# Performance work log

Hardware: AMD Instinct MI355X
Metric: run time of the kernel (lower is better)

Reference implementation:

```python
import jax, jax.numpy as jnp
import numpy as np

B, S, D, H = 2, 2048, 1024, 16
DEPTH = D // H

def setup_inputs() -> dict:
    key = jax.random.key(0)
    k1, k2, k3 = jax.random.split(key, 3)
    x = jax.random.normal(k1, (B, S, D), dtype=jnp.float32)
    # causal mask (1 = attend, 0 = blocked), broadcastable over batch/heads
    mask = jnp.tril(jnp.ones((S, S), dtype=jnp.int32))[None, None]
    W_qkv = jax.random.normal(k2, (D, 3 * D), dtype=jnp.float32) * (D ** -0.5)
    b_qkv = jnp.zeros((3 * D,), dtype=jnp.float32)
    W_out = jax.random.normal(k3, (D, D), dtype=jnp.float32) * (D ** -0.5)
    b_out = jnp.zeros((D,), dtype=jnp.float32)
    return {"x": x, "mask": mask, "W_qkv": W_qkv, "b_qkv": b_qkv,
            "W_out": W_out, "b_out": b_out}

def reference(x, mask, W_qkv, b_qkv, W_out, b_out):
    b, s, _ = x.shape
    qkv = x @ W_qkv + b_qkv                        # [b, s, 3D]
    qkv = qkv.reshape(b, s, H, 3 * DEPTH)          # matches torch reshape
    qkv = jnp.transpose(qkv, (0, 2, 1, 3))         # [b, h, s, 3*depth]
    q, k, v = jnp.split(qkv, 3, axis=-1)           # each [b, h, s, depth]
    scores = jnp.einsum('bhqd,bhkd->bhqk', q, k) / jnp.sqrt(jnp.float32(DEPTH))
    scores = jnp.where(mask == 0, -jnp.inf, scores)
    attn = jax.nn.softmax(scores, axis=-1)         # dropout: eval mode (identity)
    out = jnp.einsum('bhqk,bhkd->bhqd', attn, v)   # [b, h, s, depth]
    out = jnp.transpose(out, (0, 2, 1, 3)).reshape(b, s, D)
    return out @ W_out + b_out
```

## Files before the change

kernel.cpp:

```cpp
#include <hip/hip_runtime.h>

#define BB 2
#define SS 2048
#define DDIM 1024
#define HH 16
#define DEPTH 64
#define QKVN (3*DDIM)

typedef unsigned short u16;
typedef unsigned int u32;
typedef __attribute__((ext_vector_type(8))) short bf16x8;
typedef __attribute__((ext_vector_type(4))) float f32x4;

__device__ __forceinline__ u16 f2bf(float f){
  union{float f; u32 u;} z; z.f=f;
  u32 r = z.u + 0x7fffu + ((z.u>>16)&1u);
  return (u16)(r>>16);
}
#define NEG_BIG (-1e30f)

typedef const __attribute__((address_space(1))) u32* gas_t;
typedef __attribute__((address_space(3))) u32* las_t;
__device__ __forceinline__ void gl_lds16(const void* g, void* l){
  __builtin_amdgcn_global_load_lds((gas_t)g, (las_t)l, 16, 0, 0);
}

__global__ void convT_k(const float* __restrict__ in, u16* __restrict__ out, int R, int C){
  __shared__ float tile[32][33];
  int c0 = blockIdx.x<<5, r0 = blockIdx.y<<5;
  int tx = threadIdx.x, ty = threadIdx.y;
  for (int i=ty;i<32;i+=8) tile[i][tx] = in[(size_t)(r0+i)*C + c0+tx];
  __syncthreads();
  for (int i=ty;i<32;i+=8) out[(size_t)(c0+i)*R + r0+tx] = f2bf(tile[tx][i]);
}

__global__ void convX_k(const float* __restrict__ in, u16* __restrict__ out){
  size_t i = ((size_t)blockIdx.x*256 + threadIdx.x) * 8;
  float4 a = *(const float4*)(in + i);
  float4 b = *(const float4*)(in + i + 4);
  ushort4 lo = { f2bf(a.x), f2bf(a.y), f2bf(a.z), f2bf(a.w) };
  ushort4 hi = { f2bf(b.x), f2bf(b.y), f2bf(b.z), f2bf(b.w) };
  *(ushort4*)(out + i)     = lo;
  *(ushort4*)(out + i + 4) = hi;
}

__global__ __launch_bounds__(256,2) void gemm_qkv_k(
    const u16* __restrict__ A, const u16* __restrict__ Bt,
    const float* __restrict__ bias,
    u16* __restrict__ Qb, u16* __restrict__ Kb, u16* __restrict__ Vt)
{
  const int K = DDIM;
  __shared__ __align__(16) u16 As[128*32];
  __shared__ __align__(16) u16 Bs[128*32];
  const int tid = threadIdx.x;
  const int m0 = blockIdx.x<<7, n0 = blockIdx.y<<7;
  const int w = tid>>6, lane = tid&63, q = lane>>4, ln = lane&15;
  const int wr = (w>>1)<<6, wc = (w&1)<<6;

  f32x4 acc[4][4];
  #pragma unroll
  for (int i=0;i<4;i++)
    #pragma unroll
    for (int j=0;j<4;j++) acc[i][j] = (f32x4){0.f,0.f,0.f,0.f};

  for (int k0=0;k0<K;k0+=32){
    {
      int c = tid, row = c>>2, off = (c&3)<<3;
      gl_lds16(&A [(size_t)(m0+row)*K + k0 + off], &As[c<<3]);
      gl_lds16(&Bt[(size_t)(n0+row)*K + k0 + off], &Bs[c<<3]);
      c = tid + 256; row = c>>2; off = (c&3)<<3;
      gl_lds16(&A [(size_t)(m0+row)*K + k0 + off], &As[c<<3]);
      gl_lds16(&Bt[(size_t)(n0+row)*K + k0 + off], &Bs[c<<3]);
    }
    __syncthreads();
    bf16x8 af[4], bfr[4];
    #pragma unroll
    for (int i=0;i<4;i++) af[i]  = *(const bf16x8*)&As[((wr + (i<<4) + ln)<<5) + (q<<3)];
    #pragma unroll
    for (int j=0;j<4;j++) bfr[j] = *(const bf16x8*)&Bs[((wc + (j<<4) + ln)<<5) + (q<<3)];
    #pragma unroll
    for (int i=0;i<4;i++)
      #pragma unroll
      for (int j=0;j<4;j++)
        acc[i][j] = __builtin_amdgcn_mfma_f32_16x16x32_bf16(af[i], bfr[j], acc[i][j], 0, 0, 0);
    __syncthreads();
  }

  #pragma unroll
  for (int i=0;i<4;i++){
    const int mmb = m0 + wr + (i<<4) + (q<<2);
    const int bsel = mmb >> 11;
    const int sb   = mmb & 2047;
    #pragma unroll
    for (int j=0;j<4;j++){
      const int n = n0 + wc + (j<<4) + ln;
      const int h = n / 192;
      const int rr = n - h*192;
      const int bh = (bsel<<4) + h;
      const float bv = bias[n];
      if (rr < 64){
        u16* dst = Qb + (size_t)bh*SS*DEPTH + rr;
        #pragma unroll
        for (int r=0;r<4;r++) dst[(size_t)(sb+r)*DEPTH] = f2bf((acc[i][j][r] + bv)*0.125f);
      } else if (rr < 128){
        u16* dst = Kb + (size_t)bh*SS*DEPTH + (rr-64);
        #pragma unroll
        for (int r=0;r<4;r++) dst[(size_t)(sb+r)*DEPTH] = f2bf(acc[i][j][r] + bv);
      } else {
        ushort4 pv = { f2bf(acc[i][j][0] + bv), f2bf(acc[i][j][1] + bv),
                       f2bf(acc[i][j][2] + bv), f2bf(acc[i][j][3] + bv) };
        *(ushort4*)(Vt + ((size_t)bh*DEPTH + (rr-128))*SS + sb) = pv;
      }
    }
  }
}

__global__ __launch_bounds__(256,4) void attn_k(
    u16* __restrict__ Qb, const u16* __restrict__ Kb, const u16* __restrict__ Vt)
{
  __shared__ __align__(16) u16 Ks[64*64];
  __shared__ __align__(16) u16 VsT[64*64];
  __shared__ __align__(16) u16 ps[4][16*72];

  const int tid = threadIdx.x, w = tid>>6, lane = tid&63, q = lane>>4, ln = lane&15;
  const int bh = blockIdx.x;
  const int y  = blockIdx.y, sgrp = y>>3, rr_ = y&7;
  const int qt = (sgrp==0) ? 31-rr_ : (sgrp==1) ? 16+rr_ : (sgrp==2) ? 15-rr_ : rr_;
  const int r0 = qt<<6;
  const size_t kbase = (size_t)bh*SS*DEPTH;
  const size_t vbase = (size_t)bh*DEPTH*SS;

  bf16x8 qf[2];
  #pragma unroll
  for (int ks=0;ks<2;ks++)
    qf[ks] = *(const bf16x8*)(Qb + kbase + (size_t)(r0 + (w<<4) + ln)*DEPTH + (ks<<5) + (q<<3));

  f32x4 o[4];
  #pragma unroll
  for (int nt=0;nt<4;nt++) o[nt] = (f32x4){0.f,0.f,0.f,0.f};
  float m_r[4], l_r[4];
  #pragma unroll
  for (int r=0;r<4;r++){ m_r[r] = NEG_BIG; l_r[r] = 0.f; }

  const int T = qt + 1;
  for (int t=0;t<T;t++){
    __syncthreads();
    #pragma unroll
    for (int p=0;p<2;p++){
      const int e = (p*256 + tid)*8;
      gl_lds16(Kb + kbase + (size_t)(t<<6)*DEPTH + e, &Ks[e]);
      const int j = e>>6, d = e&63;
      gl_lds16(Vt + vbase + (size_t)j*SS + (t<<6) + d, &VsT[e]);
    }
    __syncthreads();

    f32x4 sc[4];
    #pragma unroll
    for (int jt=0;jt<4;jt++) sc[jt] = (f32x4){0.f,0.f,0.f,0.f};
    #pragma unroll
    for (int ks=0;ks<2;ks++){
      #pragma unroll
      for (int jt=0;jt<4;jt++){
        bf16x8 kf = *(const bf16x8*)&Ks[(((jt<<4)+ln)<<6) + (ks<<5) + (q<<3)];
        sc[jt] = __builtin_amdgcn_mfma_f32_16x16x32_bf16(qf[ks], kf, sc[jt], 0, 0, 0);
      }
    }

    if (t == T-1){
      const int rowb = r0 + (w<<4) + (q<<2);
      #pragma unroll
      for (int jt=0;jt<4;jt++){
        const int col = (t<<6) + (jt<<4) + ln;
        #pragma unroll
        for (int r=0;r<4;r++)
          if (col > rowb + r) sc[jt][r] = NEG_BIG;
      }
    }

    float alpha_r[4];
    #pragma unroll
    for (int r=0;r<4;r++){
      float mt = fmaxf(fmaxf(sc[0][r], sc[1][r]), fmaxf(sc[2][r], sc[3][r]));
      #pragma unroll
      for (int off=1; off<16; off<<=1) mt = fmaxf(mt, __shfl_xor(mt, off));
      const float mnew = fmaxf(m_r[r], mt);
      alpha_r[r] = __expf(m_r[r] - mnew);
      float p0 = __expf(sc[0][r]-mnew), p1 = __expf(sc[1][r]-mnew);
      float p2 = __expf(sc[2][r]-mnew), p3 = __expf(sc[3][r]-mnew);
      const int mrow = (q<<2) + r;
      ps[w][mrow*72 +      ln] = f2bf(p0);
      ps[w][mrow*72 + 16 + ln] = f2bf(p1);
      ps[w][mrow*72 + 32 + ln] = f2bf(p2);
      ps[w][mrow*72 + 48 + ln] = f2bf(p3);
      float psum = (p0+p1)+(p2+p3);
      #pragma unroll
      for (int off=1; off<16; off<<=1) psum += __shfl_xor(psum, off);
      l_r[r] = l_r[r]*alpha_r[r] + psum;
      m_r[r] = mnew;
    }
    #pragma unroll
    for (int nt=0;nt<4;nt++)
      #pragma unroll
      for (int r=0;r<4;r++) o[nt][r] *= alpha_r[r];

    __syncthreads();

    #pragma unroll
    for (int ks=0;ks<2;ks++){
      bf16x8 pa = *(const bf16x8*)&ps[w][ln*72 + (ks<<5) + (q<<3)];
      #pragma unroll
      for (int nt=0;nt<4;nt++){
        bf16x8 vf = *(const bf16x8*)&VsT[(((nt<<4)+ln)<<6) + (ks<<5) + (q<<3)];
        o[nt] = __builtin_amdgcn_mfma_f32_16x16x32_bf16(pa, vf, o[nt], 0, 0, 0);
      }
    }
  }

  #pragma unroll
  for (int r=0;r<4;r++){
    const float rl = 1.f / fmaxf(l_r[r], 1e-30f);
    const int s = r0 + (w<<4) + (q<<2) + r;
    #pragma unroll
    for (int nt=0;nt<4;nt++)
      Qb[kbase + (size_t)s*DEPTH + (nt<<4) + ln] = f2bf(o[nt][r] * rl);
  }
}

__global__ __launch_bounds__(256,2) void gemm_out_k(
    const u16* __restrict__ Aq, const u16* __restrict__ Bt,
    const float* __restrict__ bias, float* __restrict__ out)
{
  const int K = DDIM;
  __shared__ __align__(16) u16 As[128*32];
  __shared__ __align__(16) u16 Bs[128*32];
  const int tid = threadIdx.x;
  const int m0 = blockIdx.x<<7, n0 = blockIdx.y<<7;
  const int bsel = m0>>11, ms = m0&2047;
  const int w = tid>>6, lane = tid&63, q = lane>>4, ln = lane&15;
  const int wr = (w>>1)<<6, wc = (w&1)<<6;

  f32x4 acc[4][4];
  #pragma unroll
  for (int i=0;i<4;i++)
    #pragma unroll
    for (int j=0;j<4;j++) acc[i][j] = (f32x4){0.f,0.f,0.f,0.f};

  for (int k0=0;k0<K;k0+=32){
    const size_t abase = (size_t)((bsel<<4) + (k0>>6))*SS*DEPTH + (k0&63);
    {
      int c = tid, row = c>>2, off = (c&3)<<3;
      gl_lds16(&Aq[abase + (size_t)(ms+row)*DEPTH + off], &As[c<<3]);
      gl_lds16(&Bt[(size_t)(n0+row)*K + k0 + off],        &Bs[c<<3]);
      c = tid + 256; row = c>>2; off = (c&3)<<3;
      gl_lds16(&Aq[abase + (size_t)(ms+row)*DEPTH + off], &As[c<<3]);
      gl_lds16(&Bt[(size_t)(n0+row)*K + k0 + off],        &Bs[c<<3]);
    }
    __syncthreads();
    bf16x8 af[4], bfr[4];
    #pragma unroll
    for (int i=0;i<4;i++) af[i]  = *(const bf16x8*)&As[((wr + (i<<4) + ln)<<5) + (q<<3)];
    #pragma unroll
    for (int j=0;j<4;j++) bfr[j] = *(const bf16x8*)&Bs[((wc + (j<<4) + ln)<<5) + (q<<3)];
    #pragma unroll
    for (int i=0;i<4;i++)
      #pragma unroll
      for (int j=0;j<4;j++)
        acc[i][j] = __builtin_amdgcn_mfma_f32_16x16x32_bf16(af[i], bfr[j], acc[i][j], 0, 0, 0);
    __syncthreads();
  }

  #pragma unroll
  for (int i=0;i<4;i++){
    #pragma unroll
    for (int j=0;j<4;j++){
      const int n = n0 + wc + (j<<4) + ln;
      const float bv = bias[n];
      #pragma unroll
      for (int r=0;r<4;r++){
        const int mm = m0 + wr + (i<<4) + (q<<2) + r;
        out[(size_t)mm*DDIM + n] = acc[i][j][r] + bv;
      }
    }
  }
}

extern "C" void kernel_launch(void* const* d_in, const int* in_sizes, int n_in,
                              void* d_out, int out_size, void* d_ws, size_t ws_size,
                              hipStream_t stream)
{
  int ix = 0, iw = 2, ibq = 3, iwo = 4, ibo = 5;
  if (n_in == 5){ iw = 1; ibq = 2; iwo = 3; ibo = 4; }
  const float* x  = (const float*)d_in[ix];
  const float* Wq = (const float*)d_in[iw];
  const float* bq = (const float*)d_in[ibq];
  const float* Wo = (const float*)d_in[iwo];
  const float* bo = (const float*)d_in[ibo];
  float* out = (float*)d_out;

  u16* ws  = (u16*)d_ws;
  u16* Wqt = ws;
  u16* Wot = Wqt + (size_t)QKVN*DDIM;
  u16* Qb  = Wot + (size_t)DDIM*DDIM;
  u16* Kb  = Qb  + (size_t)BB*HH*SS*DEPTH;
  u16* Vt  = Kb  + (size_t)BB*HH*SS*DEPTH;
  u16* xb  = Vt  + (size_t)BB*HH*SS*DEPTH;

  convT_k<<<dim3(QKVN/32, DDIM/32), dim3(32,8), 0, stream>>>(Wq, Wqt, DDIM, QKVN);
  convT_k<<<dim3(DDIM/32, DDIM/32), dim3(32,8), 0, stream>>>(Wo, Wot, DDIM, DDIM);
  convX_k<<<dim3(BB*SS*DDIM/2048), 256, 0, stream>>>(x, xb);

  gemm_qkv_k<<<dim3(BB*SS/128, QKVN/128), 256, 0, stream>>>(xb, Wqt, bq, Qb, Kb, Vt);
  attn_k    <<<dim3(BB*HH, 32),           256, 0, stream>>>(Qb, Kb, Vt);
  gemm_out_k<<<dim3(BB*SS/128, DDIM/128), 256, 0, stream>>>(Qb, Wot, bo, out);
}
```

Before: 241.6 us.

## Fuse x conversion into QKV GEMM and prefetch K/V tiles in attention

Removes the separate fp32-to-bf16 conversion kernel for x by converting inside the QKV GEMM's A-tile load. In attention, the next K/V tile is prefetched into registers while the current one is computed, and LDS rows are padded to 72 elements to reduce bank conflicts. Probability tiles are also packed two bf16 values per 32-bit store using a lane shuffle. The trade-offs are more global fp32 traffic for A in every GEMM tile (x is re-read for each N block), higher register pressure, and synchronous loads replacing the async global-to-LDS copies.

```diff
diff --git a/kernel.cpp b/kernel.cpp
--- a/kernel.cpp
+++ b/kernel.cpp
@@ -34,18 +34,8 @@
   for (int i=ty;i<32;i+=8) out[(size_t)(c0+i)*R + r0+tx] = f2bf(tile[tx][i]);
 }
 
-__global__ void convX_k(const float* __restrict__ in, u16* __restrict__ out){
-  size_t i = ((size_t)blockIdx.x*256 + threadIdx.x) * 8;
-  float4 a = *(const float4*)(in + i);
-  float4 b = *(const float4*)(in + i + 4);
-  ushort4 lo = { f2bf(a.x), f2bf(a.y), f2bf(a.z), f2bf(a.w) };
-  ushort4 hi = { f2bf(b.x), f2bf(b.y), f2bf(b.z), f2bf(b.w) };
-  *(ushort4*)(out + i)     = lo;
-  *(ushort4*)(out + i + 4) = hi;
-}
-
 __global__ __launch_bounds__(256,2) void gemm_qkv_k(
-    const u16* __restrict__ A, const u16* __restrict__ Bt,
+    const float* __restrict__ Xf, const u16* __restrict__ Bt,
     const float* __restrict__ bias,
     u16* __restrict__ Qb, u16* __restrict__ Kb, u16* __restrict__ Vt)
 {
@@ -64,12 +54,15 @@
     for (int j=0;j<4;j++) acc[i][j] = (f32x4){0.f,0.f,0.f,0.f};
 
   for (int k0=0;k0<K;k0+=32){
-    {
-      int c = tid, row = c>>2, off = (c&3)<<3;
-      gl_lds16(&A [(size_t)(m0+row)*K + k0 + off], &As[c<<3]);
-      gl_lds16(&Bt[(size_t)(n0+row)*K + k0 + off], &Bs[c<<3]);
-      c = tid + 256; row = c>>2; off = (c&3)<<3;
-      gl_lds16(&A [(size_t)(m0+row)*K + k0 + off], &As[c<<3]);
+    #pragma unroll
+    for (int p=0;p<2;p++){
+      const int c = tid + (p<<8), row = c>>2, off = (c&3)<<3;
+      const float* ap = Xf + (size_t)(m0+row)*K + k0 + off;
+      float4 a0 = *(const float4*)ap, a1 = *(const float4*)(ap+4);
+      ushort4 lo = { f2bf(a0.x), f2bf(a0.y), f2bf(a0.z), f2bf(a0.w) };
+      ushort4 hi = { f2bf(a1.x), f2bf(a1.y), f2bf(a1.z), f2bf(a1.w) };
+      *(ushort4*)&As[c<<3]       = lo;
+      *(ushort4*)&As[(c<<3) + 4] = hi;
       gl_lds16(&Bt[(size_t)(n0+row)*K + k0 + off], &Bs[c<<3]);
     }
     __syncthreads();
@@ -118,8 +111,8 @@
 __global__ __launch_bounds__(256,4) void attn_k(
     u16* __restrict__ Qb, const u16* __restrict__ Kb, const u16* __restrict__ Vt)
 {
-  __shared__ __align__(16) u16 Ks[64*64];
-  __shared__ __align__(16) u16 VsT[64*64];
+  __shared__ __align__(16) u16 Ks[64*72];
+  __shared__ __align__(16) u16 VsT[64*72];
   __shared__ __align__(16) u16 ps[4][16*72];
 
   const int tid = threadIdx.x, w = tid>>6, lane = tid&63, q = lane>>4, ln = lane&15;
@@ -142,17 +135,36 @@
   #pragma unroll
   for (int r=0;r<4;r++){ m_r[r] = NEG_BIG; l_r[r] = 0.f; }
 
+  uint4 kreg[2], vreg[2];
+  #pragma unroll
+  for (int p=0;p<2;p++){
+    const int e = (p*256 + tid)*8;
+    const int j = e>>6, d = e&63;
+    kreg[p] = *(const uint4*)(Kb + kbase + e);
+    vreg[p] = *(const uint4*)(Vt + vbase + (size_t)j*SS + d);
+  }
+
   const int T = qt + 1;
   for (int t=0;t<T;t++){
     __syncthreads();
     #pragma unroll
     for (int p=0;p<2;p++){
       const int e = (p*256 + tid)*8;
-      gl_lds16(Kb + kbase + (size_t)(t<<6)*DEPTH + e, &Ks[e]);
       const int j = e>>6, d = e&63;
-      gl_lds16(Vt + vbase + (size_t)j*SS + (t<<6) + d, &VsT[e]);
-    }
-    __syncthreads();
+      *(uint4*)&Ks[j*72 + d]  = kreg[p];
+      *(uint4*)&VsT[j*72 + d] = vreg[p];
+    }
+    __syncthreads();
+
+    if (t+1 < T){
+      #pragma unroll
+      for (int p=0;p<2;p++){
+        const int e = (p*256 + tid)*8;
+        const int j = e>>6, d = e&63;
+        kreg[p] = *(const uint4*)(Kb + kbase + (size_t)((t+1)<<6)*DEPTH + e);
+        vreg[p] = *(const uint4*)(Vt + vbase + (size_t)j*SS + ((t+1)<<6) + d);
+      }
+    }
 
     f32x4 sc[4];
     #pragma unroll
@@ -161,7 +173,7 @@
     for (int ks=0;ks<2;ks++){
       #pragma unroll
       for (int jt=0;jt<4;jt++){
-        bf16x8 kf = *(const bf16x8*)&Ks[(((jt<<4)+ln)<<6) + (ks<<5) + (q<<3)];
+        bf16x8 kf = *(const bf16x8*)&Ks[((jt<<4)+ln)*72 + (ks<<5) + (q<<3)];
         sc[jt] = __builtin_amdgcn_mfma_f32_16x16x32_bf16(qf[ks], kf, sc[jt], 0, 0, 0);
       }
     }
@@ -185,14 +197,17 @@
       for (int off=1; off<16; off<<=1) mt = fmaxf(mt, __shfl_xor(mt, off));
       const float mnew = fmaxf(m_r[r], mt);
       alpha_r[r] = __expf(m_r[r] - mnew);
-      float p0 = __expf(sc[0][r]-mnew), p1 = __expf(sc[1][r]-mnew);
-      float p2 = __expf(sc[2][r]-mnew), p3 = __expf(sc[3][r]-mnew);
       const int mrow = (q<<2) + r;
-      ps[w][mrow*72 +      ln] = f2bf(p0);
-      ps[w][mrow*72 + 16 + ln] = f2bf(p1);
-      ps[w][mrow*72 + 32 + ln] = f2bf(p2);
-      ps[w][mrow*72 + 48 + ln] = f2bf(p3);
-      float psum = (p0+p1)+(p2+p3);
+      float psum = 0.f;
+      #pragma unroll
+      for (int jt=0;jt<4;jt++){
+        const float p = __expf(sc[jt][r] - mnew);
+        psum += p;
+        const u32 myv = (u32)f2bf(p);
+        const u32 ov  = __shfl_xor(myv, 1);
+        if ((ln & 1) == 0)
+          *(u32*)&ps[w][mrow*72 + (jt<<4) + ln] = myv | (ov<<16);
+      }
       #pragma unroll
       for (int off=1; off<16; off<<=1) psum += __shfl_xor(psum, off);
       l_r[r] = l_r[r]*alpha_r[r] + psum;
@@ -210,7 +225,7 @@
       bf16x8 pa = *(const bf16x8*)&ps[w][ln*72 + (ks<<5) + (q<<3)];
       #pragma unroll
       for (int nt=0;nt<4;nt++){
-        bf16x8 vf = *(const bf16x8*)&VsT[(((nt<<4)+ln)<<6) + (ks<<5) + (q<<3)];
+        bf16x8 vf = *(const bf16x8*)&VsT[((nt<<4)+ln)*72 + (ks<<5) + (q<<3)];
         o[nt] = __builtin_amdgcn_mfma_f32_16x16x32_bf16(pa, vf, o[nt], 0, 0, 0);
       }
     }
@@ -303,13 +318,11 @@
   u16* Qb  = Wot + (size_t)DDIM*DDIM;
   u16* Kb  = Qb  + (size_t)BB*HH*SS*DEPTH;
   u16* Vt  = Kb  + (size_t)BB*HH*SS*DEPTH;
-  u16* xb  = Vt  + (size_t)BB*HH*SS*DEPTH;
 
   convT_k<<<dim3(QKVN/32, DDIM/32), dim3(32,8), 0, stream>>>(Wq, Wqt, DDIM, QKVN);
   convT_k<<<dim3(DDIM/32, DDIM/32), dim3(32,8), 0, stream>>>(Wo, Wot, DDIM, DDIM);
-  convX_k<<<dim3(BB*SS*DDIM/2048), 256, 0, stream>>>(x, xb);
-
-  gemm_qkv_k<<<dim3(BB*SS/128, QKVN/128), 256, 0, stream>>>(xb, Wqt, bq, Qb, Kb, Vt);
+
+  gemm_qkv_k<<<dim3(BB*SS/128, QKVN/128), 256, 0, stream>>>(x, Wqt, bq, Qb, Kb, Vt);
   attn_k    <<<dim3(BB*HH, 32),           256, 0, stream>>>(Qb, Kb, Vt);
   gemm_out_k<<<dim3(BB*SS/128, DDIM/128), 256, 0, stream>>>(Qb, Wot, bo, out);
 }
```

After: 281.1 us. 1.16x slower.
